# Optimization experiments

Measured on AMD Instinct MI355X. Metric: run time of the kernel, lower is better.

## Reference

```python
import jax, jax.numpy as jnp
import numpy as np

B, C, H, W = 8, 64, 64, 64
CK = C // 8  # query/key channels

def setup_inputs() -> dict:
    key = jax.random.key(0)
    ks = jax.random.split(key, 8)
    x = jax.random.normal(ks[0], (B, C, H, W), dtype=jnp.float32)
    # Conv1d with kernel size 1 == per-position linear map; store weights as [out, in].
    # (Spectral norm only rescales the weight matrix; with given weights the forward
    #  math is an ordinary 1x1 conv.)
    Wq = jax.random.normal(ks[1], (CK, C), dtype=jnp.float32) / np.sqrt(C)
    bq = jnp.zeros((CK,), dtype=jnp.float32)
    Wk = jax.random.normal(ks[2], (CK, C), dtype=jnp.float32) / np.sqrt(C)
    bk = jnp.zeros((CK,), dtype=jnp.float32)
    Wv = jax.random.normal(ks[3], (C, C), dtype=jnp.float32) / np.sqrt(C)
    bv = jnp.zeros((C,), dtype=jnp.float32)
    gamma = jnp.asarray(0.5, dtype=jnp.float32)  # nonzero so attention path matters
    return {"x": x, "Wq": Wq, "bq": bq, "Wk": Wk, "bk": bk, "Wv": Wv, "bv": bv, "gamma": gamma}

def reference(x, Wq, bq, Wk, bk, Wv, bv, gamma):
    b, c, h, w = x.shape
    flat = x.reshape(b, c, h * w)                       # [B, C, L]
    q = jnp.einsum('oc,bcl->blo', Wq, flat) + bq        # [B, L, C/8] (query permuted)
    k = jnp.einsum('oc,bcl->bol', Wk, flat) + bk[None, :, None]   # [B, C/8, L]
    v = jnp.einsum('oc,bcl->bol', Wv, flat) + bv[None, :, None]   # [B, C, L]
    qk = jnp.einsum('blo,bom->blm', q, k)               # [B, L, L]
    attn = jax.nn.softmax(qk, axis=1)                   # softmax over dim 1 (rows)
    out = jnp.einsum('bcl,blm->bcm', v, attn)           # [B, C, L]
    out = out.reshape(b, c, h, w)
    return gamma * out + x
```

## Files before the change

### kernel.cpp

```cpp
#include <hip/hip_runtime.h>
#include <math.h>

#define B_   8
#define C_   64
#define CK_  8
#define L_   4096

typedef __attribute__((ext_vector_type(8))) __bf16 bf16x8;
typedef __attribute__((ext_vector_type(4))) __bf16 bf16x4;
typedef __attribute__((ext_vector_type(4))) float  f32x4;

__global__ __launch_bounds__(256) void qkv_kernel(
    const float* __restrict__ x,
    const float* __restrict__ Wq, const float* __restrict__ bq,
    const float* __restrict__ Wk, const float* __restrict__ bk,
    const float* __restrict__ Wv, const float* __restrict__ bv,
    __bf16* __restrict__ qo, __bf16* __restrict__ ko, __bf16* __restrict__ vpack)
{
    __shared__ float LWq[CK_ * C_];
    __shared__ float LWk[CK_ * C_];
    __shared__ float LWv[C_ * C_];
    __shared__ float LX[64][68];
    __shared__ __bf16 Lqs[64 * 8];
    __shared__ __bf16 Lks[64 * 8];

    const int tid = threadIdx.x;
    const int b  = blockIdx.x >> 6;
    const int t  = blockIdx.x & 63;
    const int l0 = t << 6;

    if (tid < 128) {
        ((float4*)LWq)[tid] = ((const float4*)Wq)[tid];
        ((float4*)LWk)[tid] = ((const float4*)Wk)[tid];
    }
    #pragma unroll
    for (int j = 0; j < 4; ++j)
        ((float4*)LWv)[tid + j * 256] = ((const float4*)Wv)[tid + j * 256];
    {
        const int c = tid >> 2, part = tid & 3;
        const float* xrow = x + ((size_t)b * C_ + c) * L_ + l0 + part * 16;
        float4* dst = (float4*)&LX[c][part * 16];
        #pragma unroll
        for (int u = 0; u < 4; ++u) dst[u] = ((const float4*)xrow)[u];
    }
    __syncthreads();

    const int lg = tid & 15;
    const int g  = tid >> 4;

    float va[4][4];
    float qk[4];
    #pragma unroll
    for (int j = 0; j < 4; ++j) {
        float bb = bv[4 * g + j];
        va[j][0] = bb; va[j][1] = bb; va[j][2] = bb; va[j][3] = bb;
    }
    {
        float bb = (g < 8) ? bq[g] : bk[g - 8];
        qk[0] = bb; qk[1] = bb; qk[2] = bb; qk[3] = bb;
    }
    const float* wqk = (g < 8) ? (LWq + g * C_) : (LWk + (g - 8) * C_);

    #pragma unroll 4
    for (int c4 = 0; c4 < 16; ++c4) {
        float4 xv[4];
        #pragma unroll
        for (int u = 0; u < 4; ++u)
            xv[u] = *(const float4*)&LX[4 * c4 + u][lg * 4];
        #pragma unroll
        for (int j = 0; j < 4; ++j) {
            float4 wv = ((const float4*)(LWv + (4 * g + j) * C_))[c4];
            float* a = va[j];
            a[0]=fmaf(wv.x,xv[0].x,a[0]); a[1]=fmaf(wv.x,xv[0].y,a[1]); a[2]=fmaf(wv.x,xv[0].z,a[2]); a[3]=fmaf(wv.x,xv[0].w,a[3]);
            a[0]=fmaf(wv.y,xv[1].x,a[0]); a[1]=fmaf(wv.y,xv[1].y,a[1]); a[2]=fmaf(wv.y,xv[1].z,a[2]); a[3]=fmaf(wv.y,xv[1].w,a[3]);
            a[0]=fmaf(wv.z,xv[2].x,a[0]); a[1]=fmaf(wv.z,xv[2].y,a[1]); a[2]=fmaf(wv.z,xv[2].z,a[2]); a[3]=fmaf(wv.z,xv[2].w,a[3]);
            a[0]=fmaf(wv.w,xv[3].x,a[0]); a[1]=fmaf(wv.w,xv[3].y,a[1]); a[2]=fmaf(wv.w,xv[3].z,a[2]); a[3]=fmaf(wv.w,xv[3].w,a[3]);
        }
        {
            float4 wv = ((const float4*)wqk)[c4];
            qk[0]=fmaf(wv.x,xv[0].x,qk[0]); qk[1]=fmaf(wv.x,xv[0].y,qk[1]); qk[2]=fmaf(wv.x,xv[0].z,qk[2]); qk[3]=fmaf(wv.x,xv[0].w,qk[3]);
            qk[0]=fmaf(wv.y,xv[1].x,qk[0]); qk[1]=fmaf(wv.y,xv[1].y,qk[1]); qk[2]=fmaf(wv.y,xv[1].z,qk[2]); qk[3]=fmaf(wv.y,xv[1].w,qk[3]);
            qk[0]=fmaf(wv.z,xv[2].x,qk[0]); qk[1]=fmaf(wv.z,xv[2].y,qk[1]); qk[2]=fmaf(wv.z,xv[2].z,qk[2]); qk[3]=fmaf(wv.z,xv[2].w,qk[3]);
            qk[0]=fmaf(wv.w,xv[3].x,qk[0]); qk[1]=fmaf(wv.w,xv[3].y,qk[1]); qk[2]=fmaf(wv.w,xv[3].z,qk[2]); qk[3]=fmaf(wv.w,xv[3].w,qk[3]);
        }
    }

    {
        __bf16* vt = vpack + ((size_t)b * 64 + t) * 4096;
        const int cb = g >> 2;
        const int sg = lg >> 2;
        const int qd = lg & 3;
        #pragma unroll
        for (int j = 0; j < 4; ++j) {
            bf16x4 vv;
            vv[0]=(__bf16)va[j][0]; vv[1]=(__bf16)va[j][1]; vv[2]=(__bf16)va[j][2]; vv[3]=(__bf16)va[j][3];
            *(bf16x4*)(vt + ((size_t)((cb * 4 + sg) * 64 + qd * 16 + (g & 3) * 4 + j)) * 4) = vv;
        }
    }
    #pragma unroll
    for (int u = 0; u < 4; ++u) {
        if (g < 8) Lqs[(lg * 4 + u) * 8 + g]       = (__bf16)qk[u];
        else       Lks[(lg * 4 + u) * 8 + (g - 8)] = (__bf16)qk[u];
    }
    __syncthreads();
    if (tid < 64) {
        *(bf16x8*)(qo + ((size_t)b * L_ + l0 + tid) * 8) = *(bf16x8*)(Lqs + tid * 8);
        *(bf16x8*)(ko + ((size_t)b * L_ + l0 + tid) * 8) = *(bf16x8*)(Lks + tid * 8);
    }
}

__global__ __launch_bounds__(512, 4) void attn_kernel(
    const __bf16* __restrict__ q, const __bf16* __restrict__ kT,
    const __bf16* __restrict__ VP, const float* __restrict__ x,
    const float* __restrict__ gamma_p, float* __restrict__ out)
{
    __shared__ __bf16 Lv[2][4][4096];
    __shared__ float  csA[8][16];

    const int tid  = threadIdx.x;
    const int w    = tid >> 6;
    const int lane = tid & 63;
    const int quad = lane >> 4;
    const int l16  = lane & 15;
    const int wh   = w & 3;
    const int lh   = w >> 2;
    const int wg   = blockIdx.x;
    const int b    = wg & 7;
    const int mb   = wg >> 3;
    const int m0   = mb << 6;

    const __bf16* vp = VP + (size_t)b * (64 * 4096);
    const __bf16* qb = q  + (size_t)b * L_ * CK_;

    bf16x8 kf = {};
    if (quad == 0) kf = *(const bf16x8*)(kT + ((size_t)b * L_ + m0 + wh * 16 + l16) * CK_);

    const __bf16* gk[4];
    int ok[4];
    #pragma unroll
    for (int k = 0; k < 4; ++k) {
        const int u = w * 4 + k, tl = u >> 3, seg = u & 7;
        gk[k] = vp + (size_t)((tl & 1) * 32 + (tl >> 1)) * 4096 + seg * 512 + lane * 8;
        ok[k] = tl * 4096 + seg * 512 + lane * 8;
    }

    f32x4 acc[4] = {};
    float csum = 0.f;
    bf16x8 r[4];

    #pragma unroll
    for (int k = 0; k < 4; ++k) r[k] = *(const bf16x8*)gk[k];
    #pragma unroll
    for (int k = 0; k < 4; ++k) *(bf16x8*)(&Lv[0][0][0] + ok[k]) = r[k];

    for (int i = 0; i < 16; ++i) {
        __syncthreads();

        if (i < 15) {
            #pragma unroll
            for (int k = 0; k < 4; ++k)
                r[k] = *(const bf16x8*)(gk[k] + (size_t)(i + 1) * 8192);
        }

        bf16x8 qA[4], qB[4];
        #pragma unroll
        for (int sg = 0; sg < 4; ++sg) {
            qA[sg] = *(const bf16x8*)(qb + (size_t)((lh * 32 + 2 * i)     * 64 + sg * 16 + l16) * CK_);
            qB[sg] = *(const bf16x8*)(qb + (size_t)((lh * 32 + 2 * i + 1) * 64 + sg * 16 + l16) * CK_);
        }

        bf16x4 pkA[4], pkB[4];
        #pragma unroll
        for (int sg = 0; sg < 4; ++sg) {
            f32x4 sv = __builtin_amdgcn_mfma_f32_16x16x32_bf16(qA[sg], kf, (f32x4){0.f,0.f,0.f,0.f}, 0, 0, 0);
            const float e0 = __expf(sv[0]);
            const float e1 = __expf(sv[1]);
            const float e2 = __expf(sv[2]);
            const float e3 = __expf(sv[3]);
            csum += (e0 + e1) + (e2 + e3);
            pkA[sg][0]=(__bf16)e0; pkA[sg][1]=(__bf16)e1; pkA[sg][2]=(__bf16)e2; pkA[sg][3]=(__bf16)e3;
        }
        #pragma unroll
        for (int sg = 0; sg < 4; ++sg) {
            f32x4 sv = __builtin_amdgcn_mfma_f32_16x16x32_bf16(qB[sg], kf, (f32x4){0.f,0.f,0.f,0.f}, 0, 0, 0);
            const float e0 = __expf(sv[0]);
            const float e1 = __expf(sv[1]);
            const float e2 = __expf(sv[2]);
            const float e3 = __expf(sv[3]);
            csum += (e0 + e1) + (e2 + e3);
            pkB[sg][0]=(__bf16)e0; pkB[sg][1]=(__bf16)e1; pkB[sg][2]=(__bf16)e2; pkB[sg][3]=(__bf16)e3;
        }

        const __bf16* LbA = &Lv[i & 1][lh][0];
        const __bf16* LbB = &Lv[i & 1][2 + lh][0];
        #pragma unroll
        for (int sg = 0; sg < 4; ++sg) {
            bf16x8 p8 = __builtin_shufflevector(pkA[sg], pkB[sg], 0, 1, 2, 3, 4, 5, 6, 7);
            #pragma unroll
            for (int cb = 0; cb < 4; ++cb) {
                bf16x4 vfA = *(const bf16x4*)(LbA + ((size_t)((cb * 4 + sg) * 64 + lane)) * 4);
                bf16x4 vfB = *(const bf16x4*)(LbB + ((size_t)((cb * 4 + sg) * 64 + lane)) * 4);
                bf16x8 a8 = __builtin_shufflevector(vfA, vfB, 0, 1, 2, 3, 4, 5, 6, 7);
                acc[cb] = __builtin_amdgcn_mfma_f32_16x16x32_bf16(a8, p8, acc[cb], 0, 0, 0);
            }
        }

        if (i < 15) {
            const int nb = (i + 1) & 1;
            #pragma unroll
            for (int k = 0; k < 4; ++k)
                *(bf16x8*)(&Lv[nb][0][0] + ok[k]) = r[k];
        }
    }

    float* Sc = (float*)&Lv[0][0][0];
    if (lh == 1) {
        #pragma unroll
        for (int cb = 0; cb < 4; ++cb)
            #pragma unroll
            for (int r2 = 0; r2 < 4; ++r2)
                Sc[(wh * 64 + cb * 16 + quad * 4 + r2) * 16 + l16] = acc[cb][r2];
    }
    csum += __shfl_xor(csum, 16);
    csum += __shfl_xor(csum, 32);
    if (quad == 0) csA[w][l16] = csum;
    __syncthreads();

    if (lh == 0) {
        const float rinv = gamma_p[0] / (csA[wh][l16] + csA[wh + 4][l16]);
        #pragma unroll
        for (int cb = 0; cb < 4; ++cb) {
            #pragma unroll
            for (int r2 = 0; r2 < 4; ++r2) {
                const int c = cb * 16 + quad * 4 + r2;
                const float vsum = acc[cb][r2] + Sc[(wh * 64 + c) * 16 + l16];
                const size_t idx = ((size_t)(b * 64 + c)) * L_ + m0 + wh * 16 + l16;
                out[idx] = fmaf(rinv, vsum, x[idx]);
            }
        }
    }
}

extern "C" void kernel_launch(void* const* d_in, const int* in_sizes, int n_in,
                              void* d_out, int out_size, void* d_ws, size_t ws_size,
                              hipStream_t stream) {
    const float* x  = (const float*)d_in[0];
    const float* Wq = (const float*)d_in[1];
    const float* bq = (const float*)d_in[2];
    const float* Wk = (const float*)d_in[3];
    const float* bk = (const float*)d_in[4];
    const float* Wv = (const float*)d_in[5];
    const float* bv = (const float*)d_in[6];
    const float* gm = (const float*)d_in[7];
    float* out = (float*)d_out;

    __bf16* ws    = (__bf16*)d_ws;
    __bf16* qo    = ws;
    __bf16* ko    = ws + 262144;
    __bf16* vpack = ws + 524288;

    qkv_kernel<<<dim3(B_ * (L_ / 64)), dim3(256), 0, stream>>>(
        x, Wq, bq, Wk, bk, Wv, bv, qo, ko, vpack);
    attn_kernel<<<dim3(B_ * 64), dim3(512), 0, stream>>>(
        qo, ko, vpack, x, gm, out);
}
```

Measured before the change: 125.5 us.

## Interleave V pack for 16-byte LDS reads and stage Q tiles through LDS

The V tensor is repacked so the two bf16x4 halves that each MFMA A-operand needs sit next to each other. This lets the attention kernel read one bf16x8 from LDS instead of two bf16x4 loads plus a shuffle. Q tiles are now prefetched cooperatively into a double-buffered LDS array alongside V, replacing redundant per-wave global loads of Q. The cost is extra LDS capacity and some extra global loads and LDS stores in the producer loop, which may affect occupancy.

```diff
diff --git a/kernel.cpp b/kernel.cpp
--- a/kernel.cpp
+++ b/kernel.cpp
@@ -86,7 +86,8 @@
     }
 
     {
-        __bf16* vt = vpack + ((size_t)b * 64 + t) * 4096;
+        const int T = t >> 1, p = t & 1;
+        __bf16* vt = vpack + ((size_t)(b * 32 + T)) * 8192 + p * 4;
         const int cb = g >> 2;
         const int sg = lg >> 2;
         const int qd = lg & 3;
@@ -94,7 +95,7 @@
         for (int j = 0; j < 4; ++j) {
             bf16x4 vv;
             vv[0]=(__bf16)va[j][0]; vv[1]=(__bf16)va[j][1]; vv[2]=(__bf16)va[j][2]; vv[3]=(__bf16)va[j][3];
-            *(bf16x4*)(vt + ((size_t)((cb * 4 + sg) * 64 + qd * 16 + (g & 3) * 4 + j)) * 4) = vv;
+            *(bf16x4*)(vt + (size_t)((cb * 4 + sg) * 512 + (qd * 16 + (g & 3) * 4 + j) * 8)) = vv;
         }
     }
     #pragma unroll
@@ -114,7 +115,8 @@
     const __bf16* __restrict__ VP, const float* __restrict__ x,
     const float* __restrict__ gamma_p, float* __restrict__ out)
 {
-    __shared__ __bf16 Lv[2][4][4096];
+    __shared__ __bf16 Lv[2][16384];
+    __shared__ __bf16 Lq[2][2][1024];
     __shared__ float  csA[8][16];
 
     const int tid  = threadIdx.x;
@@ -129,8 +131,8 @@
     const int mb   = wg >> 3;
     const int m0   = mb << 6;
 
-    const __bf16* vp = VP + (size_t)b * (64 * 4096);
-    const __bf16* qb = q  + (size_t)b * L_ * CK_;
+    const __bf16* vp2 = VP + (size_t)b * 262144;
+    const __bf16* qb  = q  + (size_t)b * L_ * CK_;
 
     bf16x8 kf = {};
     if (quad == 0) kf = *(const bf16x8*)(kT + ((size_t)b * L_ + m0 + wh * 16 + l16) * CK_);
@@ -139,19 +141,23 @@
     int ok[4];
     #pragma unroll
     for (int k = 0; k < 4; ++k) {
-        const int u = w * 4 + k, tl = u >> 3, seg = u & 7;
-        gk[k] = vp + (size_t)((tl & 1) * 32 + (tl >> 1)) * 4096 + seg * 512 + lane * 8;
-        ok[k] = tl * 4096 + seg * 512 + lane * 8;
-    }
+        const int u = w * 4 + k, h = u >> 4, s16 = u & 15;
+        gk[k] = vp2 + (size_t)(h * 16) * 8192 + s16 * 512 + lane * 8;
+        ok[k] = h * 8192 + s16 * 512 + lane * 8;
+    }
+    const __bf16* gq = qb + (size_t)((w >> 1) * 2048 + (w & 1) * 64 + lane) * 8;
+    const int oq = (w >> 1) * 1024 + (w & 1) * 512 + lane * 8;
 
     f32x4 acc[4] = {};
     float csum = 0.f;
-    bf16x8 r[4];
+    bf16x8 r[4], rq;
 
     #pragma unroll
     for (int k = 0; k < 4; ++k) r[k] = *(const bf16x8*)gk[k];
-    #pragma unroll
-    for (int k = 0; k < 4; ++k) *(bf16x8*)(&Lv[0][0][0] + ok[k]) = r[k];
+    if (w < 4) rq = *(const bf16x8*)gq;
+    #pragma unroll
+    for (int k = 0; k < 4; ++k) *(bf16x8*)(&Lv[0][0] + ok[k]) = r[k];
+    if (w < 4) *(bf16x8*)(&Lq[0][0][0] + oq) = rq;
 
     for (int i = 0; i < 16; ++i) {
         __syncthreads();
@@ -160,13 +166,15 @@
             #pragma unroll
             for (int k = 0; k < 4; ++k)
                 r[k] = *(const bf16x8*)(gk[k] + (size_t)(i + 1) * 8192);
-        }
-
+            if (w < 4) rq = *(const bf16x8*)(gq + (size_t)(i + 1) * 1024);
+        }
+
+        const __bf16* Lqh = &Lq[i & 1][lh][0];
         bf16x8 qA[4], qB[4];
         #pragma unroll
         for (int sg = 0; sg < 4; ++sg) {
-            qA[sg] = *(const bf16x8*)(qb + (size_t)((lh * 32 + 2 * i)     * 64 + sg * 16 + l16) * CK_);
-            qB[sg] = *(const bf16x8*)(qb + (size_t)((lh * 32 + 2 * i + 1) * 64 + sg * 16 + l16) * CK_);
+            qA[sg] = *(const bf16x8*)(Lqh + (sg * 16 + l16) * 8);
+            qB[sg] = *(const bf16x8*)(Lqh + 512 + (sg * 16 + l16) * 8);
         }
 
         bf16x4 pkA[4], pkB[4];
@@ -191,16 +199,13 @@
             pkB[sg][0]=(__bf16)e0; pkB[sg][1]=(__bf16)e1; pkB[sg][2]=(__bf16)e2; pkB[sg][3]=(__bf16)e3;
         }
 
-        const __bf16* LbA = &Lv[i & 1][lh][0];
-        const __bf16* LbB = &Lv[i & 1][2 + lh][0];
+        const __bf16* Lb = &Lv[i & 1][lh * 8192];
         #pragma unroll
         for (int sg = 0; sg < 4; ++sg) {
             bf16x8 p8 = __builtin_shufflevector(pkA[sg], pkB[sg], 0, 1, 2, 3, 4, 5, 6, 7);
             #pragma unroll
             for (int cb = 0; cb < 4; ++cb) {
-                bf16x4 vfA = *(const bf16x4*)(LbA + ((size_t)((cb * 4 + sg) * 64 + lane)) * 4);
-                bf16x4 vfB = *(const bf16x4*)(LbB + ((size_t)((cb * 4 + sg) * 64 + lane)) * 4);
-                bf16x8 a8 = __builtin_shufflevector(vfA, vfB, 0, 1, 2, 3, 4, 5, 6, 7);
+                bf16x8 a8 = *(const bf16x8*)(Lb + (size_t)((cb * 4 + sg) * 512 + lane * 8));
                 acc[cb] = __builtin_amdgcn_mfma_f32_16x16x32_bf16(a8, p8, acc[cb], 0, 0, 0);
             }
         }
@@ -209,11 +214,12 @@
             const int nb = (i + 1) & 1;
             #pragma unroll
             for (int k = 0; k < 4; ++k)
-                *(bf16x8*)(&Lv[nb][0][0] + ok[k]) = r[k];
-        }
-    }
-
-    float* Sc = (float*)&Lv[0][0][0];
+                *(bf16x8*)(&Lv[nb][0] + ok[k]) = r[k];
+            if (w < 4) *(bf16x8*)(&Lq[nb][0][0] + oq) = rq;
+        }
+    }
+
+    float* Sc = (float*)&Lv[0][0];
     if (lh == 1) {
         #pragma unroll
         for (int cb = 0; cb < 4; ++cb)
```

After: 119.1 us. 5.1% less time.
